# Optimization experiments

Hardware: AMD Instinct MI355X
Metric: run time of the kernel (lower is better)

The kernel has to match this reference:

```python
import jax, jax.numpy as jnp
import numpy as np

# Dims: tokens [B,H,W,C]; 3x3 local window (NB=9 neighbors); relative-pos embed dim RP.
B, H, W, C = 4, 96, 96, 128
K, NB, RP = 3, 9, 8
HID = 128              # edge_hidden_dim = max(hidden_dim//2=128, feature_dim=128)
EDGE_IN = 3 * C + RP   # [center, neighbor, center-neighbor, rel_pos] -> 392
CLIP = 3.0
GATE_EPS = 1e-6
LN_EPS = 1e-5


def _ln(x, w, b):
    m = jnp.mean(x, axis=-1, keepdims=True)
    v = jnp.mean((x - m) ** 2, axis=-1, keepdims=True)
    return (x - m) * jax.lax.rsqrt(v + LN_EPS) * w + b


def _mlp(x, w1, b1, w2, b2):
    # Linear -> GELU (exact/erf, torch default) -> Linear; dropout is identity in eval mode.
    return jax.nn.gelu(x @ w1 + b1, approximate=False) @ w2 + b2


def _eml(drive, resistance, gamma_raw, lam, bias, warmup_eta):
    # EMLUnit energy gate (source not provided; Ohm's-law style drive/resistance,
    # positive resistance via softplus, clipped, warmup-scaled, learned bias).
    gamma = jax.nn.softplus(gamma_raw)
    conduct = drive / (jax.nn.softplus(resistance) + gamma + GATE_EPS)
    return warmup_eta * jnp.clip(lam * conduct, -CLIP, CLIP) + bias


def setup_inputs() -> dict:
    key = jax.random.key(0)
    ks = jax.random.split(key, 8)

    def w(k, shape, std=0.01):
        return jax.random.normal(k, shape, jnp.float32) * std

    return {
        "tokens": jax.random.normal(ks[0], (B, H, W, C), jnp.float32),
        "ln1_w": jnp.ones((C,), jnp.float32), "ln1_b": jnp.zeros((C,), jnp.float32),
        "ln2_w": jnp.ones((C,), jnp.float32), "ln2_b": jnp.zeros((C,), jnp.float32),
        "rel_pos": w(ks[1], (NB, RP), 0.02),
        "d_w1": w(ks[2], (EDGE_IN, HID)), "d_b1": jnp.zeros((HID,), jnp.float32),
        "d_w2": w(ks[3], (HID, 1)), "d_b2": jnp.zeros((1,), jnp.float32),
        "r_w1": w(ks[4], (EDGE_IN, HID)), "r_b1": jnp.zeros((HID,), jnp.float32),
        "r_w2": w(ks[5], (HID, 1)), "r_b2": jnp.zeros((1,), jnp.float32),
        "v_w": w(ks[6], (C, C)), "v_b": jnp.zeros((C,), jnp.float32),
        "o_w": w(ks[7], (C, C)), "o_b": jnp.zeros((C,), jnp.float32),
        "eml_gamma": jnp.full((1,), 0.1, jnp.float32),
        "eml_lam": jnp.ones((1,), jnp.float32),
        "eml_bias": jnp.full((1,), -0.3, jnp.float32),
    }


def reference(tokens, ln1_w, ln1_b, ln2_w, ln2_b, rel_pos,
              d_w1, d_b1, d_w2, d_b2, r_w1, r_b1, r_w2, r_b2,
              v_w, v_b, o_w, o_b, eml_gamma, eml_lam, eml_bias):
    b, h, w_, c = tokens.shape
    hw = h * w_
    norm = _ln(tokens, ln1_w, ln1_b)
    # nn.Unfold(kernel=3, padding=1): zero-pad then gather 3x3 windows (row-major ky,kx order).
    pad = jnp.pad(norm, ((0, 0), (1, 1), (1, 1), (0, 0)))
    neigh = jnp.stack([pad[:, dy:dy + h, dx:dx + w_, :]
                       for dy in range(K) for dx in range(K)], axis=3)  # [B,H,W,9,C]
    neigh = neigh.reshape(b, hw, NB, c)
    center = jnp.broadcast_to(norm.reshape(b, hw, 1, c), (b, hw, NB, c))
    relp = jnp.broadcast_to(rel_pos[None, None], (b, hw, NB, RP))
    edge = jnp.concatenate([center, neigh, center - neigh, relp], axis=-1)  # [B,HW,9,392]
    drive = _mlp(edge, d_w1, d_b1, d_w2, d_b2)[..., 0]        # [B,HW,9]
    resistance = _mlp(edge, r_w1, r_b1, r_w2, r_b2)[..., 0]   # [B,HW,9]
    energy = _eml(drive, resistance, eml_gamma, eml_lam, eml_bias, 1.0)
    gate = jax.nn.sigmoid(energy)[..., None]                  # [B,HW,9,1]
    values = neigh @ v_w + v_b                                # [B,HW,9,C]
    gate_mass = jnp.clip(jnp.sum(gate, axis=2), GATE_EPS, None)  # [B,HW,1]
    message = jnp.sum(gate * values, axis=2) / gate_mass      # [B,HW,C]
    update = (message @ o_w + o_b).reshape(b, h, w_, c)
    return _ln(tokens + update, ln2_w, ln2_b)
```

## Files before the change

kernel.cpp:

```cpp
#include <hip/hip_runtime.h>
#include <stdint.h>

#define NPIX 36864

using bf16x8 = __attribute__((ext_vector_type(8))) short;
using f32x4  = __attribute__((ext_vector_type(4))) float;
using f32x2  = __attribute__((ext_vector_type(2))) float;

__device__ __forceinline__ float bf2f(uint16_t u){
  return __uint_as_float(((uint32_t)u) << 16);
}
__device__ __forceinline__ float bl(uint32_t u){ return __uint_as_float(u << 16); }
__device__ __forceinline__ float bh(uint32_t u){ return __uint_as_float(u & 0xFFFF0000u); }
__device__ __forceinline__ uint16_t f2bf(float f){
  uint32_t u = __float_as_uint(f);
  u += 0x7fffu + ((u >> 16) & 1u);
  return (uint16_t)(u >> 16);
}
__device__ __forceinline__ float ldw(const void* p, int i, bool f32){
  return f32 ? ((const float*)p)[i] : bf2f(((const uint16_t*)p)[i]);
}
__device__ __forceinline__ bool probe_f32(const void* ones_vec){
  return ((const uint32_t*)ones_vec)[0] == 0x3F800000u;
}
__device__ __forceinline__ float softplusf(float x){
  return fmaxf(x, 0.f) + __logf(1.f + __expf(-fabsf(x)));
}
__device__ __forceinline__ f32x2 up2(uint32_t u){
  f32x2 r; r.x = __uint_as_float(u << 16); r.y = __uint_as_float(u & 0xFFFF0000u); return r;
}
__device__ __forceinline__ void sg2(f32x2& acc, uint32_t c, uint32_t n, f32x2 r, f32x2 w){
  f32x2 z = up2(c) + up2(n) + r;
  float sx = __builtin_amdgcn_fmed3f(fmaf(z.x, 0.4255f, 0.5f), 0.f, 1.f);
  float sy = __builtin_amdgcn_fmed3f(fmaf(z.y, 0.4255f, 0.5f), 0.f, 1.f);
  acc.x = fmaf(z.x * sx, w.x, acc.x);
  acc.y = fmaf(z.y * sy, w.y, acc.y);
}

#define LIDX(p, ch) ((p)*128 + ((((ch) >> 3) ^ ((p) & 15)) << 3) + ((ch) & 7))

__global__ __launch_bounds__(256) void pre_kernel(const void* __restrict__ tokens,
                            const void* __restrict__ ln1w, const void* __restrict__ ln1b,
                            const void* __restrict__ dw1, const void* __restrict__ rw1,
                            const void* __restrict__ vw,  const void* __restrict__ relp,
                            const void* __restrict__ db1, const void* __restrict__ rb1,
                            const void* __restrict__ ow,
                            const void* __restrict__ dw2, const void* __restrict__ rw2,
                            const void* __restrict__ vb,  const void* __restrict__ db2,
                            const void* __restrict__ rb2, const void* __restrict__ eg,
                            const void* __restrict__ el,  const void* __restrict__ eb,
                            uint16_t* __restrict__ norm,
                            uint16_t* __restrict__ wcatT, float* __restrict__ Rd,
                            float* __restrict__ Rr, uint16_t* __restrict__ owT,
                            float* __restrict__ w2df, float* __restrict__ w2rf,
                            float* __restrict__ vbf, float* __restrict__ sc){
  const bool F = probe_f32(ln1w);
  const int b = blockIdx.x;
  if (b < NPIX/4){
    const int wv = threadIdx.x >> 6, lane = threadIdx.x & 63;
    const int p = b * 4 + wv;
    float f0, f1;
    if (F){
      const float2 t = ((const float2*)tokens)[(size_t)p*64 + lane];
      f0 = t.x; f1 = t.y;
    } else {
      const uint32_t pk = ((const uint32_t*)tokens)[(size_t)p*64 + lane];
      f0 = bl(pk); f1 = bh(pk);
    }
    float s = f0 + f1;
    #pragma unroll
    for (int m = 1; m < 64; m <<= 1) s += __shfl_xor(s, m, 64);
    const float mean = s * (1.f/128.f);
    const float d0 = f0 - mean, d1 = f1 - mean;
    float q = d0*d0 + d1*d1;
    #pragma unroll
    for (int m = 1; m < 64; m <<= 1) q += __shfl_xor(q, m, 64);
    const float rs = rsqrtf(q * (1.f/128.f) + 1e-5f);
    const float n0 = d0*rs*ldw(ln1w, 2*lane, F)   + ldw(ln1b, 2*lane, F);
    const float n1 = d1*rs*ldw(ln1w, 2*lane+1, F) + ldw(ln1b, 2*lane+1, F);
    ((uint32_t*)(norm + (size_t)p*128))[lane] = (uint32_t)f2bf(n0) | ((uint32_t)f2bf(n1) << 16);
    return;
  }
  const int j = (b - NPIX/4) * 2 + (threadIdx.x >> 7);
  const int c = threadIdx.x & 127;
  if (j < 640){
    float val;
    if (j < 128)      val = ldw(dw1, c*128 + j, F)             + ldw(dw1, (256+c)*128 + j, F);
    else if (j < 256) val = ldw(dw1, (128+c)*128 + (j-128), F) - ldw(dw1, (256+c)*128 + (j-128), F);
    else if (j < 384) val = ldw(rw1, c*128 + (j-256), F)       + ldw(rw1, (256+c)*128 + (j-256), F);
    else if (j < 512) val = ldw(rw1, (128+c)*128 + (j-384), F) - ldw(rw1, (256+c)*128 + (j-384), F);
    else              val = ldw(vw, c*128 + (j-512), F);
    wcatT[j*128 + c] = f2bf(val);
  } else if (j < 649){
    const int k = j - 640;
    float sd = ldw(db1, c, F);
    float sr = ldw(rb1, c, F);
    #pragma unroll
    for (int r = 0; r < 8; ++r){
      float rp = ldw(relp, k*8 + r, F);
      sd += rp * ldw(dw1, (384+r)*128 + c, F);
      sr += rp * ldw(rw1, (384+r)*128 + c, F);
    }
    Rd[k*128 + c] = sd;
    Rr[k*128 + c] = sr;
  } else if (j < 777){
    const int n = j - 649;
    owT[n*128 + c] = f2bf(ldw(ow, c*128 + n, F));
  } else {
    w2df[c] = ldw(dw2, c, F);
    w2rf[c] = ldw(rw2, c, F);
    vbf[c]  = ldw(vb, c, F);
    if (c == 0){
      sc[0] = ldw(db2, 0, F);
      sc[1] = ldw(rb2, 0, F);
      sc[2] = softplusf(ldw(eg, 0, F));
      sc[3] = ldw(el, 0, F);
      sc[4] = ldw(eb, 0, F);
    }
  }
}

__global__ __launch_bounds__(512, 4) void mega_kernel(
    const uint16_t* __restrict__ norm, const uint16_t* __restrict__ wcatT,
    const uint16_t* __restrict__ owT,
    const float* __restrict__ Rd, const float* __restrict__ Rr,
    const float* __restrict__ w2df, const float* __restrict__ w2rf,
    const float* __restrict__ sc, const float* __restrict__ vbf,
    const void* __restrict__ tokens, const void* __restrict__ ob,
    const void* __restrict__ ln2w, const void* __restrict__ ln2b,
    void* __restrict__ out){
  __shared__ __align__(16) char smem[78336];
  uint16_t* const Ns = (uint16_t*)smem;
  uint16_t* const PA = (uint16_t*)(smem + 28672);
  uint16_t* const PB = (uint16_t*)(smem + 57344);
  float*    const drv = (float*)(smem + 73728);
  float*    const gts = (float*)(smem + 76032);
  float*    const U   = (float*)smem;

  const int bid0 = blockIdx.x;
  const int bid  = (bid0 & 7)*72 + (bid0 >> 3);
  const int b  = bid / 144;
  const int tl = bid - b*144;
  const int ty = tl / 12;
  const int y0 = ty*8, x0 = (tl - ty*12)*8;
  const int tid = threadIdx.x;
  const int wv = tid >> 6, lane = tid & 63;
  const int lr = lane & 15, quad = lane >> 4;
  const float sc0 = sc[0], sc1 = sc[1], sc2 = sc[2], sc3 = sc[3], sc4 = sc[4];

  #pragma unroll
  for (int i = 0; i < 4; ++i){
    const int idx = tid + i*512;
    if (idx < 1792){
      const int hq = idx >> 4, g = idx & 15;
      uint4 v = {0u,0u,0u,0u};
      if (hq < 100){
        const int hy = hq/10, hx = hq - hy*10;
        const int y = y0 - 1 + hy, x = x0 - 1 + hx;
        if (((unsigned)y < 96u) && ((unsigned)x < 96u))
          v = *(const uint4*)&norm[((size_t)((b*96+y)*96+x))*128 + g*8];
      }
      *(uint4*)&Ns[hq*128 + ((g ^ (hq & 15)) << 3)] = v;
    }
  }

  auto loadB = [&](const uint16_t* __restrict__ Wp, bf16x8 (&bfr)[4]){
    const uint16_t* base = Wp + (size_t)(wv*16 + lr)*128 + quad*8;
    #pragma unroll
    for (int kk = 0; kk < 4; ++kk)
      bfr[kk] = *(const bf16x8*)(base + kk*32);
  };

  auto gemmH = [&](const uint16_t* __restrict__ Wp){
    bf16x8 bfr[4];
    loadB(Wp, bfr);
    f32x4 acc[7] = {};
    #pragma unroll
    for (int kk = 0; kk < 4; ++kk){
      const int chunk = kk*4 + quad;
      #pragma unroll
      for (int mi = 0; mi < 7; ++mi){
        const int r = mi*16 + lr;
        const bf16x8 a = *(const bf16x8*)&Ns[r*128 + ((chunk ^ (r & 15)) << 3)];
        acc[mi] = __builtin_amdgcn_mfma_f32_16x16x32_bf16(a, bfr[kk], acc[mi], 0, 0, 0);
      }
    }
    const int col = wv*16 + lr;
    #pragma unroll
    for (int mi = 0; mi < 7; ++mi){
      const int rowb = mi*16 + quad*4;
      #pragma unroll
      for (int r = 0; r < 4; ++r)
        PA[LIDX(rowb + r, col)] = f2bf(acc[mi][r]);
    }
  };

  auto gemmC = [&](const uint16_t* __restrict__ Wp){
    bf16x8 bfr[4];
    loadB(Wp, bfr);
    f32x4 acc[4] = {};
    #pragma unroll
    for (int kk = 0; kk < 4; ++kk){
      const int chunk = kk*4 + quad;
      #pragma unroll
      for (int mi = 0; mi < 4; ++mi){
        const int r = mi*16 + lr;
        const int hr = (r >> 3)*10 + (r & 7) + 11;
        const bf16x8 a = *(const bf16x8*)&Ns[hr*128 + ((chunk ^ (hr & 15)) << 3)];
        acc[mi] = __builtin_amdgcn_mfma_f32_16x16x32_bf16(a, bfr[kk], acc[mi], 0, 0, 0);
      }
    }
    const int col = wv*16 + lr;
    #pragma unroll
    for (int mi = 0; mi < 4; ++mi){
      const int rowb = mi*16 + quad*4;
      #pragma unroll
      for (int r = 0; r < 4; ++r)
        PB[LIDX(rowb + r, col)] = f2bf(acc[mi][r]);
    }
  };

  auto edge = [&](const float* __restrict__ Rk, const float* __restrict__ w2, bool isDrive){
    const int pl = lane >> 3, cg = lane & 7;
    for (int i = 0; i < 9; ++i){
      const int it = wv*9 + i;
      const int k = it >> 3, ry = it & 7;
      const int ky = k/3, kx = k - ky*3;
      const int pr = ry*8 + pl;
      const int hq = (ry + ky)*10 + pl + kx;
      const int g0 = 2*cg;
      const uint4 c0 = *(const uint4*)((const char*)PB + pr*256 + (((g0)  ^ (pr & 15)) << 4));
      const uint4 c1 = *(const uint4*)((const char*)PB + pr*256 + (((g0+1)^ (pr & 15)) << 4));
      const uint4 n0 = *(const uint4*)((const char*)PA + hq*256 + (((g0)  ^ (hq & 15)) << 4));
      const uint4 n1 = *(const uint4*)((const char*)PA + hq*256 + (((g0+1)^ (hq & 15)) << 4));
      const float4* r4 = (const float4*)(Rk + k*128) + cg*4;
      const float4* w4 = (const float4*)w2 + cg*4;
      const float4 Ra = r4[0], Rb = r4[1], Rc = r4[2], Rv = r4[3];
      const float4 Wa = w4[0], Wb = w4[1], Wc = w4[2], Wd = w4[3];
      f32x2 a = {0.f, 0.f};
      sg2(a, c0.x, n0.x, f32x2{Ra.x, Ra.y}, f32x2{Wa.x, Wa.y});
      sg2(a, c0.y, n0.y, f32x2{Ra.z, Ra.w}, f32x2{Wa.z, Wa.w});
      sg2(a, c0.z, n0.z, f32x2{Rb.x, Rb.y}, f32x2{Wb.x, Wb.y});
      sg2(a, c0.w, n0.w, f32x2{Rb.z, Rb.w}, f32x2{Wb.z, Wb.w});
      sg2(a, c1.x, n1.x, f32x2{Rc.x, Rc.y}, f32x2{Wc.x, Wc.y});
      sg2(a, c1.y, n1.y, f32x2{Rc.z, Rc.w}, f32x2{Wc.z, Wc.w});
      sg2(a, c1.z, n1.z, f32x2{Rv.x, Rv.y}, f32x2{Wd.x, Wd.y});
      sg2(a, c1.w, n1.w, f32x2{Rv.z, Rv.w}, f32x2{Wd.z, Wd.w});
      float s = a.x + a.y;
      s += __shfl_xor(s, 1, 64); s += __shfl_xor(s, 2, 64); s += __shfl_xor(s, 4, 64);
      if (cg == 0){
        if (isDrive){
          drv[k*64 + pr] = s;
        } else {
          const float drive  = drv[k*64 + pr] + sc0;
          const float resist = s + sc1;
          const float cond = __fdividef(drive, softplusf(resist) + sc2 + 1e-6f);
          const float en = fminf(fmaxf(sc3 * cond, -3.0f), 3.0f) + sc4;
          const float e = __expf(-en);
          gts[k*64 + pr] = __builtin_amdgcn_rcpf(1.0f + e);
        }
      }
    }
  };

  const uint16_t* const W0 = wcatT;
  const uint16_t* const W1 = wcatT + (size_t)1*128*128;
  const uint16_t* const W2 = wcatT + (size_t)2*128*128;
  const uint16_t* const W3 = wcatT + (size_t)3*128*128;
  const uint16_t* const W4 = wcatT + (size_t)4*128*128;

  __syncthreads();
  gemmH(W1); gemmC(W0);
  __syncthreads();
  edge(Rd, w2df, true);
  __syncthreads();
  gemmH(W3); gemmC(W2);
  __syncthreads();
  edge(Rr, w2rf, false);
  __syncthreads();
  gemmH(W4);
  __syncthreads();

  {
    const float2 vb2 = ((const float2*)vbf)[lane];
    const int g = lane >> 2, lb = (lane & 3)*4;
    #pragma unroll
    for (int j = 0; j < 8; ++j){
      const int mp = wv*8 + j;
      const int my = mp >> 3, mx = mp & 7;
      float gk[9], gsum = 0.f;
      #pragma unroll
      for (int kk = 0; kk < 9; ++kk){ gk[kk] = gts[kk*64 + mp]; gsum += gk[kk]; }
      float a0 = 0.f, a1 = 0.f;
      #pragma unroll
      for (int kk = 0; kk < 9; ++kk){
        const int kyy = kk / 3;
        const int h2  = (my + kyy)*10 + (mx + kk - kyy*3);
        const uint32_t u = *(const uint32_t*)((const char*)PA + h2*256 + ((g ^ (h2 & 15)) << 4) + lb);
        a0 = fmaf(gk[kk], bl(u), a0);
        a1 = fmaf(gk[kk], bh(u), a1);
      }
      const float inv = __fdividef(1.0f, fmaxf(gsum, 1e-6f));
      a0 = (a0 + gsum * vb2.x) * inv;
      a1 = (a1 + gsum * vb2.y) * inv;
      *(uint32_t*)((char*)PB + mp*256 + ((g ^ (mp & 15)) << 4) + lb) =
          (uint32_t)f2bf(a0) | ((uint32_t)f2bf(a1) << 16);
    }
  }
  __syncthreads();

  f32x4 acc[4] = {};
  {
    bf16x8 bfr[4];
    loadB(owT, bfr);
    #pragma unroll
    for (int kk = 0; kk < 4; ++kk){
      const int chunk = kk*4 + quad;
      #pragma unroll
      for (int mi = 0; mi < 4; ++mi){
        const int r = mi*16 + lr;
        const bf16x8 a = *(const bf16x8*)&PB[r*128 + ((chunk ^ (r & 15)) << 3)];
        acc[mi] = __builtin_amdgcn_mfma_f32_16x16x32_bf16(a, bfr[kk], acc[mi], 0, 0, 0);
      }
    }
  }
  __syncthreads();
  {
    const int col = wv*16 + lr;
    #pragma unroll
    for (int mi = 0; mi < 4; ++mi)
      #pragma unroll
      for (int r = 0; r < 4; ++r)
        U[(mi*16 + quad*4 + r)*128 + col] = acc[mi][r];
  }
  __syncthreads();

  const bool F = probe_f32(ln2w);
  const float lw0 = ldw(ln2w, 2*lane, F), lw1 = ldw(ln2w, 2*lane+1, F);
  const float lb0 = ldw(ln2b, 2*lane, F), lb1 = ldw(ln2b, 2*lane+1, F);
  const float ob0 = ldw(ob, 2*lane, F),   ob1 = ldw(ob, 2*lane+1, F);
  #pragma unroll
  for (int j = 0; j < 8; ++j){
    const int row = wv*8 + j;
    const int my = row >> 3, mx = row & 7;
    const size_t p = (size_t)((b*96 + y0 + my)*96 + (x0 + mx));
    const float2 uv = ((const float2*)U)[row*64 + lane];
    float t0, t1;
    if (F){
      const float2 tk = ((const float2*)tokens)[p*64 + lane];
      t0 = tk.x; t1 = tk.y;
    } else {
      const uint32_t tk = ((const uint32_t*)tokens)[p*64 + lane];
      t0 = bl(tk); t1 = bh(tk);
    }
    const float a0 = uv.x + ob0 + t0;
    const float a1 = uv.y + ob1 + t1;
    float s = a0 + a1;
    #pragma unroll
    for (int m = 1; m < 64; m <<= 1) s += __shfl_xor(s, m, 64);
    const float mean = s * (1.f/128.f);
    const float d0 = a0 - mean, d1 = a1 - mean;
    float q = d0*d0 + d1*d1;
    #pragma unroll
    for (int m = 1; m < 64; m <<= 1) q += __shfl_xor(q, m, 64);
    const float rs = rsqrtf(q * (1.f/128.f) + 1e-5f);
    const float o0 = d0*rs*lw0 + lb0;
    const float o1 = d1*rs*lw1 + lb1;
    if (F){
      ((float2*)out)[p*64 + lane] = make_float2(o0, o1);
    } else {
      ((uint32_t*)out)[p*64 + lane] = (uint32_t)f2bf(o0) | ((uint32_t)f2bf(o1) << 16);
    }
  }
}

extern "C" void kernel_launch(void* const* d_in, const int* in_sizes, int n_in,
                              void* d_out, int out_size, void* d_ws, size_t ws_size,
                              hipStream_t stream) {
  const void* tokens = d_in[0];
  const void* ln1w   = d_in[1];
  const void* ln1b   = d_in[2];
  const void* ln2w   = d_in[3];
  const void* ln2b   = d_in[4];
  const void* relp   = d_in[5];
  const void* dw1    = d_in[6];
  const void* db1    = d_in[7];
  const void* dw2    = d_in[8];
  const void* db2    = d_in[9];
  const void* rw1    = d_in[10];
  const void* rb1    = d_in[11];
  const void* rw2    = d_in[12];
  const void* rb2    = d_in[13];
  const void* vw     = d_in[14];
  const void* vb     = d_in[15];
  const void* ow     = d_in[16];
  const void* ob     = d_in[17];
  const void* eg     = d_in[18];
  const void* el     = d_in[19];
  const void* eb     = d_in[20];

  char* ws = (char*)d_ws;
  uint16_t* normb = (uint16_t*)(ws + 0);
  uint16_t* wcatT = (uint16_t*)(ws + 9437184);
  float*    Rd    = (float*)   (ws + 9601024);
  float*    Rr    = (float*)   (ws + 9605632);
  uint16_t* owT   = (uint16_t*)(ws + 9610240);
  float*    w2df  = (float*)   (ws + 9643008);
  float*    w2rf  = (float*)   (ws + 9643520);
  float*    vbf   = (float*)   (ws + 9644032);
  float*    sc    = (float*)   (ws + 9644544);

  pre_kernel<<<NPIX/4 + 389, 256, 0, stream>>>(tokens, ln1w, ln1b,
                                       dw1, rw1, vw, relp, db1, rb1, ow,
                                       dw2, rw2, vb, db2, rb2, eg, el, eb,
                                       normb, wcatT, Rd, Rr, owT, w2df, w2rf, vbf, sc);
  mega_kernel<<<576, 512, 0, stream>>>(normb, wcatT, owT, Rd, Rr, w2df, w2rf,
                                       sc, vbf, tokens, ob, ln2w, ln2b, d_out);
}
```

Measured before the change: 187.5 us.

## Halve spatial tile to 4x8 pixels with 256-thread blocks and 2-column-tile waves

Shrinks each block's tile from 8x8 to 4x8 pixels and uses 256 threads instead of 512, doubling the grid to 1152 blocks. LDS use drops from about 78 KB to about 43 KB per block. Each wave now computes two 16-column MFMA tiles, reusing each A fragment across both. The aim is more resident blocks and better load balance across CUs, at the cost of a larger halo fraction (6x10 halo rows for 32 pixels) and more redundant neighbor GEMM work per pixel.

```diff
diff --git a/kernel.cpp b/kernel.cpp
--- a/kernel.cpp
+++ b/kernel.cpp
@@ -120,7 +120,7 @@
   }
 }
 
-__global__ __launch_bounds__(512, 4) void mega_kernel(
+__global__ __launch_bounds__(256, 3) void mega_kernel(
     const uint16_t* __restrict__ norm, const uint16_t* __restrict__ wcatT,
     const uint16_t* __restrict__ owT,
     const float* __restrict__ Rd, const float* __restrict__ Rr,
@@ -129,20 +129,20 @@
     const void* __restrict__ tokens, const void* __restrict__ ob,
     const void* __restrict__ ln2w, const void* __restrict__ ln2b,
     void* __restrict__ out){
-  __shared__ __align__(16) char smem[78336];
+  __shared__ __align__(16) char smem[43264];
   uint16_t* const Ns = (uint16_t*)smem;
-  uint16_t* const PA = (uint16_t*)(smem + 28672);
-  uint16_t* const PB = (uint16_t*)(smem + 57344);
-  float*    const drv = (float*)(smem + 73728);
-  float*    const gts = (float*)(smem + 76032);
+  uint16_t* const PA = (uint16_t*)(smem + 16384);
+  uint16_t* const PB = (uint16_t*)(smem + 32768);
+  float*    const drv = (float*)(smem + 40960);
+  float*    const gts = (float*)(smem + 42112);
   float*    const U   = (float*)smem;
 
   const int bid0 = blockIdx.x;
-  const int bid  = (bid0 & 7)*72 + (bid0 >> 3);
-  const int b  = bid / 144;
-  const int tl = bid - b*144;
+  const int bid  = (bid0 & 7)*144 + (bid0 >> 3);
+  const int b  = bid / 288;
+  const int tl = bid - b*288;
   const int ty = tl / 12;
-  const int y0 = ty*8, x0 = (tl - ty*12)*8;
+  const int y0 = ty*4, x0 = (tl - ty*12)*8;
   const int tid = threadIdx.x;
   const int wv = tid >> 6, lane = tid & 63;
   const int lr = lane & 15, quad = lane >> 4;
@@ -150,73 +150,84 @@
 
   #pragma unroll
   for (int i = 0; i < 4; ++i){
-    const int idx = tid + i*512;
-    if (idx < 1792){
-      const int hq = idx >> 4, g = idx & 15;
-      uint4 v = {0u,0u,0u,0u};
-      if (hq < 100){
-        const int hy = hq/10, hx = hq - hy*10;
-        const int y = y0 - 1 + hy, x = x0 - 1 + hx;
-        if (((unsigned)y < 96u) && ((unsigned)x < 96u))
-          v = *(const uint4*)&norm[((size_t)((b*96+y)*96+x))*128 + g*8];
-      }
-      *(uint4*)&Ns[hq*128 + ((g ^ (hq & 15)) << 3)] = v;
-    }
-  }
-
-  auto loadB = [&](const uint16_t* __restrict__ Wp, bf16x8 (&bfr)[4]){
-    const uint16_t* base = Wp + (size_t)(wv*16 + lr)*128 + quad*8;
-    #pragma unroll
-    for (int kk = 0; kk < 4; ++kk)
-      bfr[kk] = *(const bf16x8*)(base + kk*32);
+    const int idx = tid + i*256;
+    const int hq = idx >> 4, g = idx & 15;
+    uint4 v = {0u,0u,0u,0u};
+    if (hq < 60){
+      const int hy = hq/10, hx = hq - hy*10;
+      const int y = y0 - 1 + hy, x = x0 - 1 + hx;
+      if (((unsigned)y < 96u) && ((unsigned)x < 96u))
+        v = *(const uint4*)&norm[((size_t)((b*96+y)*96+x))*128 + g*8];
+    }
+    *(uint4*)&Ns[hq*128 + ((g ^ (hq & 15)) << 3)] = v;
+  }
+
+  auto loadB = [&](const uint16_t* __restrict__ Wp, bf16x8 (&bfr)[2][4]){
+    #pragma unroll
+    for (int ni = 0; ni < 2; ++ni){
+      const uint16_t* base = Wp + (size_t)(wv*32 + ni*16 + lr)*128 + quad*8;
+      #pragma unroll
+      for (int kk = 0; kk < 4; ++kk)
+        bfr[ni][kk] = *(const bf16x8*)(base + kk*32);
+    }
   };
 
   auto gemmH = [&](const uint16_t* __restrict__ Wp){
-    bf16x8 bfr[4];
+    bf16x8 bfr[2][4];
     loadB(Wp, bfr);
-    f32x4 acc[7] = {};
+    f32x4 acc[4][2] = {};
     #pragma unroll
     for (int kk = 0; kk < 4; ++kk){
       const int chunk = kk*4 + quad;
       #pragma unroll
-      for (int mi = 0; mi < 7; ++mi){
+      for (int mi = 0; mi < 4; ++mi){
         const int r = mi*16 + lr;
         const bf16x8 a = *(const bf16x8*)&Ns[r*128 + ((chunk ^ (r & 15)) << 3)];
-        acc[mi] = __builtin_amdgcn_mfma_f32_16x16x32_bf16(a, bfr[kk], acc[mi], 0, 0, 0);
-      }
-    }
-    const int col = wv*16 + lr;
-    #pragma unroll
-    for (int mi = 0; mi < 7; ++mi){
-      const int rowb = mi*16 + quad*4;
-      #pragma unroll
-      for (int r = 0; r < 4; ++r)
-        PA[LIDX(rowb + r, col)] = f2bf(acc[mi][r]);
+        #pragma unroll
+        for (int ni = 0; ni < 2; ++ni)
+          acc[mi][ni] = __builtin_amdgcn_mfma_f32_16x16x32_bf16(a, bfr[ni][kk], acc[mi][ni], 0, 0, 0);
+      }
+    }
+    #pragma unroll
+    for (int mi = 0; mi < 4; ++mi){
+      #pragma unroll
+      for (int ni = 0; ni < 2; ++ni){
+        const int ch   = wv*32 + ni*16 + lr;
+        const int rowb = mi*16 + quad*4;
+        #pragma unroll
+        for (int r = 0; r < 4; ++r)
+          PA[LIDX(rowb + r, ch)] = f2bf(acc[mi][ni][r]);
+      }
     }
   };
 
   auto gemmC = [&](const uint16_t* __restrict__ Wp){
-    bf16x8 bfr[4];
+    bf16x8 bfr[2][4];
     loadB(Wp, bfr);
-    f32x4 acc[4] = {};
+    f32x4 acc[2][2] = {};
     #pragma unroll
     for (int kk = 0; kk < 4; ++kk){
       const int chunk = kk*4 + quad;
       #pragma unroll
-      for (int mi = 0; mi < 4; ++mi){
+      for (int mi = 0; mi < 2; ++mi){
         const int r = mi*16 + lr;
         const int hr = (r >> 3)*10 + (r & 7) + 11;
         const bf16x8 a = *(const bf16x8*)&Ns[hr*128 + ((chunk ^ (hr & 15)) << 3)];
-        acc[mi] = __builtin_amdgcn_mfma_f32_16x16x32_bf16(a, bfr[kk], acc[mi], 0, 0, 0);
-      }
-    }
-    const int col = wv*16 + lr;
-    #pragma unroll
-    for (int mi = 0; mi < 4; ++mi){
-      const int rowb = mi*16 + quad*4;
-      #pragma unroll
-      for (int r = 0; r < 4; ++r)
-        PB[LIDX(rowb + r, col)] = f2bf(acc[mi][r]);
+        #pragma unroll
+        for (int ni = 0; ni < 2; ++ni)
+          acc[mi][ni] = __builtin_amdgcn_mfma_f32_16x16x32_bf16(a, bfr[ni][kk], acc[mi][ni], 0, 0, 0);
+      }
+    }
+    #pragma unroll
+    for (int mi = 0; mi < 2; ++mi){
+      #pragma unroll
+      for (int ni = 0; ni < 2; ++ni){
+        const int ch   = wv*32 + ni*16 + lr;
+        const int rowb = mi*16 + quad*4;
+        #pragma unroll
+        for (int r = 0; r < 4; ++r)
+          PB[LIDX(rowb + r, ch)] = f2bf(acc[mi][ni][r]);
+      }
     }
   };
 
@@ -224,7 +235,7 @@
     const int pl = lane >> 3, cg = lane & 7;
     for (int i = 0; i < 9; ++i){
       const int it = wv*9 + i;
-      const int k = it >> 3, ry = it & 7;
+      const int k = it >> 2, ry = it & 3;
       const int ky = k/3, kx = k - ky*3;
       const int pr = ry*8 + pl;
       const int hq = (ry + ky)*10 + pl + kx;
@@ -250,14 +261,14 @@
       s += __shfl_xor(s, 1, 64); s += __shfl_xor(s, 2, 64); s += __shfl_xor(s, 4, 64);
       if (cg == 0){
         if (isDrive){
-          drv[k*64 + pr] = s;
+          drv[k*32 + pr] = s;
         } else {
-          const float drive  = drv[k*64 + pr] + sc0;
+          const float drive  = drv[k*32 + pr] + sc0;
           const float resist = s + sc1;
           const float cond = __fdividef(drive, softplusf(resist) + sc2 + 1e-6f);
           const float en = fminf(fmaxf(sc3 * cond, -3.0f), 3.0f) + sc4;
           const float e = __expf(-en);
-          gts[k*64 + pr] = __builtin_amdgcn_rcpf(1.0f + e);
+          gts[k*32 + pr] = __builtin_amdgcn_rcpf(1.0f + e);
         }
       }
     }
@@ -290,7 +301,7 @@
       const int my = mp >> 3, mx = mp & 7;
       float gk[9], gsum = 0.f;
       #pragma unroll
-      for (int kk = 0; kk < 9; ++kk){ gk[kk] = gts[kk*64 + mp]; gsum += gk[kk]; }
+      for (int kk = 0; kk < 9; ++kk){ gk[kk] = gts[kk*32 + mp]; gsum += gk[kk]; }
       float a0 = 0.f, a1 = 0.f;
       #pragma unroll
       for (int kk = 0; kk < 9; ++kk){
@@ -309,29 +320,34 @@
   }
   __syncthreads();
 
-  f32x4 acc[4] = {};
+  f32x4 acc[2][2] = {};
   {
-    bf16x8 bfr[4];
+    bf16x8 bfr[2][4];
     loadB(owT, bfr);
     #pragma unroll
     for (int kk = 0; kk < 4; ++kk){
       const int chunk = kk*4 + quad;
       #pragma unroll
-      for (int mi = 0; mi < 4; ++mi){
+      for (int mi = 0; mi < 2; ++mi){
         const int r = mi*16 + lr;
         const bf16x8 a = *(const bf16x8*)&PB[r*128 + ((chunk ^ (r & 15)) << 3)];
-        acc[mi] = __builtin_amdgcn_mfma_f32_16x16x32_bf16(a, bfr[kk], acc[mi], 0, 0, 0);
+        #pragma unroll
+        for (int ni = 0; ni < 2; ++ni)
+          acc[mi][ni] = __builtin_amdgcn_mfma_f32_16x16x32_bf16(a, bfr[ni][kk], acc[mi][ni], 0, 0, 0);
       }
     }
   }
   __syncthreads();
   {
-    const int col = wv*16 + lr;
-    #pragma unroll
-    for (int mi = 0; mi < 4; ++mi)
-      #pragma unroll
-      for (int r = 0; r < 4; ++r)
-        U[(mi*16 + quad*4 + r)*128 + col] = acc[mi][r];
+    #pragma unroll
+    for (int mi = 0; mi < 2; ++mi)
+      #pragma unroll
+      for (int ni = 0; ni < 2; ++ni){
+        const int col = wv*32 + ni*16 + lr;
+        #pragma unroll
+        for (int r = 0; r < 4; ++r)
+          U[(mi*16 + quad*4 + r)*128 + col] = acc[mi][ni][r];
+      }
   }
   __syncthreads();
 
@@ -414,6 +430,6 @@
                                        dw1, rw1, vw, relp, db1, rb1, ow,
                                        dw2, rw2, vb, db2, rb2, eg, el, eb,
                                        normb, wcatT, Rd, Rr, owT, w2df, w2rf, vbf, sc);
-  mega_kernel<<<576, 512, 0, stream>>>(normb, wcatT, owT, Rd, Rr, w2df, w2rf,
-                                       sc, vbf, tokens, ob, ln2w, ln2b, d_out);
-}
+  mega_kernel<<<1152, 256, 0, stream>>>(normb, wcatT, owT, Rd, Rr, w2df, w2rf,
+                                        sc, vbf, tokens, ob, ln2w, ln2b, d_out);
+}
```

Measured after the change: 189.0 us. No clear change (+0.8%).

## Reuse center features across neighbors in edge loop and batch LN1 pixels

Applied to the files above, without the earlier changes.

The edge stage now assigns each wave one row of 8 pixels and loops over the 9 neighbors. The center features and second-layer weights are loaded and unpacked once per wave, and the next neighbor's LDS reads are prefetched while the current one is computed. The LN1 pre-kernel handles two pixels per wave so that shuffle reductions interleave, and it launches half as many blocks. The drive and gate buffers share one LDS region, and a barrier before the U write-back is removed because U does not overlap the PB region the preceding MFMA loop reads.

```diff
diff --git a/kernel.cpp b/kernel.cpp
--- a/kernel.cpp
+++ b/kernel.cpp
@@ -29,10 +29,11 @@
 __device__ __forceinline__ f32x2 up2(uint32_t u){
   f32x2 r; r.x = __uint_as_float(u << 16); r.y = __uint_as_float(u & 0xFFFF0000u); return r;
 }
-__device__ __forceinline__ void sg2(f32x2& acc, uint32_t c, uint32_t n, f32x2 r, f32x2 w){
-  f32x2 z = up2(c) + up2(n) + r;
-  float sx = __builtin_amdgcn_fmed3f(fmaf(z.x, 0.4255f, 0.5f), 0.f, 1.f);
-  float sy = __builtin_amdgcn_fmed3f(fmaf(z.y, 0.4255f, 0.5f), 0.f, 1.f);
+__device__ __forceinline__ void sgf(f32x2& acc, f32x2 c, uint32_t n, f32x2 r, f32x2 w){
+  const f32x2 nf = up2(n);
+  f32x2 z; z.x = c.x + nf.x + r.x; z.y = c.y + nf.y + r.y;
+  const float sx = __builtin_amdgcn_fmed3f(fmaf(z.x, 0.4255f, 0.5f), 0.f, 1.f);
+  const float sy = __builtin_amdgcn_fmed3f(fmaf(z.y, 0.4255f, 0.5f), 0.f, 1.f);
   acc.x = fmaf(z.x * sx, w.x, acc.x);
   acc.y = fmaf(z.y * sy, w.y, acc.y);
 }
@@ -56,32 +57,38 @@
                             float* __restrict__ vbf, float* __restrict__ sc){
   const bool F = probe_f32(ln1w);
   const int b = blockIdx.x;
-  if (b < NPIX/4){
+  if (b < NPIX/8){
     const int wv = threadIdx.x >> 6, lane = threadIdx.x & 63;
-    const int p = b * 4 + wv;
-    float f0, f1;
+    const int p = b * 8 + wv * 2;
+    float a0, a1, c0, c1;
     if (F){
-      const float2 t = ((const float2*)tokens)[(size_t)p*64 + lane];
-      f0 = t.x; f1 = t.y;
+      const float2 ta = ((const float2*)tokens)[(size_t)p*64 + lane];
+      const float2 tb = ((const float2*)tokens)[(size_t)(p+1)*64 + lane];
+      a0 = ta.x; a1 = ta.y; c0 = tb.x; c1 = tb.y;
     } else {
-      const uint32_t pk = ((const uint32_t*)tokens)[(size_t)p*64 + lane];
-      f0 = bl(pk); f1 = bh(pk);
-    }
-    float s = f0 + f1;
-    #pragma unroll
-    for (int m = 1; m < 64; m <<= 1) s += __shfl_xor(s, m, 64);
-    const float mean = s * (1.f/128.f);
-    const float d0 = f0 - mean, d1 = f1 - mean;
-    float q = d0*d0 + d1*d1;
-    #pragma unroll
-    for (int m = 1; m < 64; m <<= 1) q += __shfl_xor(q, m, 64);
-    const float rs = rsqrtf(q * (1.f/128.f) + 1e-5f);
-    const float n0 = d0*rs*ldw(ln1w, 2*lane, F)   + ldw(ln1b, 2*lane, F);
-    const float n1 = d1*rs*ldw(ln1w, 2*lane+1, F) + ldw(ln1b, 2*lane+1, F);
-    ((uint32_t*)(norm + (size_t)p*128))[lane] = (uint32_t)f2bf(n0) | ((uint32_t)f2bf(n1) << 16);
+      const uint32_t ua = ((const uint32_t*)tokens)[(size_t)p*64 + lane];
+      const uint32_t ub = ((const uint32_t*)tokens)[(size_t)(p+1)*64 + lane];
+      a0 = bl(ua); a1 = bh(ua); c0 = bl(ub); c1 = bh(ub);
+    }
+    float sa = a0 + a1, sb = c0 + c1;
+    #pragma unroll
+    for (int m = 1; m < 64; m <<= 1){ sa += __shfl_xor(sa, m, 64); sb += __shfl_xor(sb, m, 64); }
+    const float ma = sa * (1.f/128.f), mb = sb * (1.f/128.f);
+    const float da0 = a0 - ma, da1 = a1 - ma, db0 = c0 - mb, db1 = c1 - mb;
+    float qa = da0*da0 + da1*da1, qb = db0*db0 + db1*db1;
+    #pragma unroll
+    for (int m = 1; m < 64; m <<= 1){ qa += __shfl_xor(qa, m, 64); qb += __shfl_xor(qb, m, 64); }
+    const float ra = rsqrtf(qa * (1.f/128.f) + 1e-5f);
+    const float rb = rsqrtf(qb * (1.f/128.f) + 1e-5f);
+    const float w0 = ldw(ln1w, 2*lane, F), w1 = ldw(ln1w, 2*lane+1, F);
+    const float bb0 = ldw(ln1b, 2*lane, F), bb1 = ldw(ln1b, 2*lane+1, F);
+    const float na0 = da0*ra*w0 + bb0, na1 = da1*ra*w1 + bb1;
+    const float nb0 = db0*rb*w0 + bb0, nb1 = db1*rb*w1 + bb1;
+    ((uint32_t*)(norm + (size_t)p*128))[lane]     = (uint32_t)f2bf(na0) | ((uint32_t)f2bf(na1) << 16);
+    ((uint32_t*)(norm + (size_t)(p+1)*128))[lane] = (uint32_t)f2bf(nb0) | ((uint32_t)f2bf(nb1) << 16);
     return;
   }
-  const int j = (b - NPIX/4) * 2 + (threadIdx.x >> 7);
+  const int j = (b - NPIX/8) * 2 + (threadIdx.x >> 7);
   const int c = threadIdx.x & 127;
   if (j < 640){
     float val;
@@ -129,13 +136,12 @@
     const void* __restrict__ tokens, const void* __restrict__ ob,
     const void* __restrict__ ln2w, const void* __restrict__ ln2b,
     void* __restrict__ out){
-  __shared__ __align__(16) char smem[78336];
+  __shared__ __align__(16) char smem[76032];
   uint16_t* const Ns = (uint16_t*)smem;
   uint16_t* const PA = (uint16_t*)(smem + 28672);
   uint16_t* const PB = (uint16_t*)(smem + 57344);
-  float*    const drv = (float*)(smem + 73728);
-  float*    const gts = (float*)(smem + 76032);
-  float*    const U   = (float*)smem;
+  float*    const dg = (float*)(smem + 73728);
+  float*    const U  = (float*)smem;
 
   const int bid0 = blockIdx.x;
   const int bid  = (bid0 & 7)*72 + (bid0 >> 3);
@@ -222,42 +228,49 @@
 
   auto edge = [&](const float* __restrict__ Rk, const float* __restrict__ w2, bool isDrive){
     const int pl = lane >> 3, cg = lane & 7;
-    for (int i = 0; i < 9; ++i){
-      const int it = wv*9 + i;
-      const int k = it >> 3, ry = it & 7;
-      const int ky = k/3, kx = k - ky*3;
-      const int pr = ry*8 + pl;
-      const int hq = (ry + ky)*10 + pl + kx;
-      const int g0 = 2*cg;
-      const uint4 c0 = *(const uint4*)((const char*)PB + pr*256 + (((g0)  ^ (pr & 15)) << 4));
-      const uint4 c1 = *(const uint4*)((const char*)PB + pr*256 + (((g0+1)^ (pr & 15)) << 4));
-      const uint4 n0 = *(const uint4*)((const char*)PA + hq*256 + (((g0)  ^ (hq & 15)) << 4));
-      const uint4 n1 = *(const uint4*)((const char*)PA + hq*256 + (((g0+1)^ (hq & 15)) << 4));
+    const int pr = wv*8 + pl;
+    const int g0 = 2*cg;
+    const uint4 c0 = *(const uint4*)((const char*)PB + pr*256 + (((g0)  ^ (pr & 15)) << 4));
+    const uint4 c1 = *(const uint4*)((const char*)PB + pr*256 + (((g0+1)^ (pr & 15)) << 4));
+    const f32x2 cf0 = up2(c0.x), cf1 = up2(c0.y), cf2 = up2(c0.z), cf3 = up2(c0.w);
+    const f32x2 cf4 = up2(c1.x), cf5 = up2(c1.y), cf6 = up2(c1.z), cf7 = up2(c1.w);
+    const float4* w4 = (const float4*)w2 + cg*4;
+    const float4 Wa = w4[0], Wb = w4[1], Wc = w4[2], Wd = w4[3];
+    const int h0 = wv*10 + pl;
+    uint4 n0 = *(const uint4*)((const char*)PA + h0*256 + (((g0)  ^ (h0 & 15)) << 4));
+    uint4 n1 = *(const uint4*)((const char*)PA + h0*256 + (((g0+1)^ (h0 & 15)) << 4));
+    for (int k = 0; k < 9; ++k){
+      const uint4 m0 = n0, m1 = n1;
+      if (k < 8){
+        const int k2 = k + 1;
+        const int ky2 = k2 / 3, kx2 = k2 - ky2*3;
+        const int h2 = (wv + ky2)*10 + pl + kx2;
+        n0 = *(const uint4*)((const char*)PA + h2*256 + (((g0)  ^ (h2 & 15)) << 4));
+        n1 = *(const uint4*)((const char*)PA + h2*256 + (((g0+1)^ (h2 & 15)) << 4));
+      }
       const float4* r4 = (const float4*)(Rk + k*128) + cg*4;
-      const float4* w4 = (const float4*)w2 + cg*4;
       const float4 Ra = r4[0], Rb = r4[1], Rc = r4[2], Rv = r4[3];
-      const float4 Wa = w4[0], Wb = w4[1], Wc = w4[2], Wd = w4[3];
       f32x2 a = {0.f, 0.f};
-      sg2(a, c0.x, n0.x, f32x2{Ra.x, Ra.y}, f32x2{Wa.x, Wa.y});
-      sg2(a, c0.y, n0.y, f32x2{Ra.z, Ra.w}, f32x2{Wa.z, Wa.w});
-      sg2(a, c0.z, n0.z, f32x2{Rb.x, Rb.y}, f32x2{Wb.x, Wb.y});
-      sg2(a, c0.w, n0.w, f32x2{Rb.z, Rb.w}, f32x2{Wb.z, Wb.w});
-      sg2(a, c1.x, n1.x, f32x2{Rc.x, Rc.y}, f32x2{Wc.x, Wc.y});
-      sg2(a, c1.y, n1.y, f32x2{Rc.z, Rc.w}, f32x2{Wc.z, Wc.w});
-      sg2(a, c1.z, n1.z, f32x2{Rv.x, Rv.y}, f32x2{Wd.x, Wd.y});
-      sg2(a, c1.w, n1.w, f32x2{Rv.z, Rv.w}, f32x2{Wd.z, Wd.w});
+      sgf(a, cf0, m0.x, f32x2{Ra.x, Ra.y}, f32x2{Wa.x, Wa.y});
+      sgf(a, cf1, m0.y, f32x2{Ra.z, Ra.w}, f32x2{Wa.z, Wa.w});
+      sgf(a, cf2, m0.z, f32x2{Rb.x, Rb.y}, f32x2{Wb.x, Wb.y});
+      sgf(a, cf3, m0.w, f32x2{Rb.z, Rb.w}, f32x2{Wb.z, Wb.w});
+      sgf(a, cf4, m1.x, f32x2{Rc.x, Rc.y}, f32x2{Wc.x, Wc.y});
+      sgf(a, cf5, m1.y, f32x2{Rc.z, Rc.w}, f32x2{Wc.z, Wc.w});
+      sgf(a, cf6, m1.z, f32x2{Rv.x, Rv.y}, f32x2{Wd.x, Wd.y});
+      sgf(a, cf7, m1.w, f32x2{Rv.z, Rv.w}, f32x2{Wd.z, Wd.w});
       float s = a.x + a.y;
       s += __shfl_xor(s, 1, 64); s += __shfl_xor(s, 2, 64); s += __shfl_xor(s, 4, 64);
       if (cg == 0){
         if (isDrive){
-          drv[k*64 + pr] = s;
+          dg[k*64 + pr] = s;
         } else {
-          const float drive  = drv[k*64 + pr] + sc0;
+          const float drive  = dg[k*64 + pr] + sc0;
           const float resist = s + sc1;
           const float cond = __fdividef(drive, softplusf(resist) + sc2 + 1e-6f);
           const float en = fminf(fmaxf(sc3 * cond, -3.0f), 3.0f) + sc4;
           const float e = __expf(-en);
-          gts[k*64 + pr] = __builtin_amdgcn_rcpf(1.0f + e);
+          dg[k*64 + pr] = __builtin_amdgcn_rcpf(1.0f + e);
         }
       }
     }
@@ -290,7 +303,7 @@
       const int my = mp >> 3, mx = mp & 7;
       float gk[9], gsum = 0.f;
       #pragma unroll
-      for (int kk = 0; kk < 9; ++kk){ gk[kk] = gts[kk*64 + mp]; gsum += gk[kk]; }
+      for (int kk = 0; kk < 9; ++kk){ gk[kk] = dg[kk*64 + mp]; gsum += gk[kk]; }
       float a0 = 0.f, a1 = 0.f;
       #pragma unroll
       for (int kk = 0; kk < 9; ++kk){
@@ -324,7 +337,6 @@
       }
     }
   }
-  __syncthreads();
   {
     const int col = wv*16 + lr;
     #pragma unroll
@@ -410,7 +422,7 @@
   float*    vbf   = (float*)   (ws + 9644032);
   float*    sc    = (float*)   (ws + 9644544);
 
-  pre_kernel<<<NPIX/4 + 389, 256, 0, stream>>>(tokens, ln1w, ln1b,
+  pre_kernel<<<NPIX/8 + 389, 256, 0, stream>>>(tokens, ln1w, ln1b,
                                        dw1, rw1, vw, relp, db1, rb1, ow,
                                        dw2, rw2, vb, db2, rb2, eg, el, eb,
                                        normb, wcatT, Rd, Rr, owT, w2df, w2rf, vbf, sc);
```

Measured after the change: 189.5 us. No clear change (+1.0%).

## Fuse LayerNorm1 into mega kernel and drop the normalized-token workspace

Applied to the files above, without the earlier changes.

Moves the first LayerNorm out of the pre-pass and into the main tile kernel. Each block now normalizes its own 10x10 halo directly from the tokens and writes bf16 results into shared memory. This removes the 9.4MB normalized-token write and re-read and the 9216 extra pre-kernel blocks, and shrinks the pre-kernel to weight preparation only. In exchange, halo pixels are normalized redundantly (about 1.56x recompute, with shuffle reductions per row). The change also merges the drive and gate shared buffers to cut LDS use and removes one barrier before the U store.

```diff
diff --git a/kernel.cpp b/kernel.cpp
--- a/kernel.cpp
+++ b/kernel.cpp
@@ -39,8 +39,8 @@
 
 #define LIDX(p, ch) ((p)*128 + ((((ch) >> 3) ^ ((p) & 15)) << 3) + ((ch) & 7))
 
-__global__ __launch_bounds__(256) void pre_kernel(const void* __restrict__ tokens,
-                            const void* __restrict__ ln1w, const void* __restrict__ ln1b,
+__global__ __launch_bounds__(256) void pre_kernel(
+                            const void* __restrict__ ln1w,
                             const void* __restrict__ dw1, const void* __restrict__ rw1,
                             const void* __restrict__ vw,  const void* __restrict__ relp,
                             const void* __restrict__ db1, const void* __restrict__ rb1,
@@ -49,39 +49,12 @@
                             const void* __restrict__ vb,  const void* __restrict__ db2,
                             const void* __restrict__ rb2, const void* __restrict__ eg,
                             const void* __restrict__ el,  const void* __restrict__ eb,
-                            uint16_t* __restrict__ norm,
                             uint16_t* __restrict__ wcatT, float* __restrict__ Rd,
                             float* __restrict__ Rr, uint16_t* __restrict__ owT,
                             float* __restrict__ w2df, float* __restrict__ w2rf,
                             float* __restrict__ vbf, float* __restrict__ sc){
   const bool F = probe_f32(ln1w);
-  const int b = blockIdx.x;
-  if (b < NPIX/4){
-    const int wv = threadIdx.x >> 6, lane = threadIdx.x & 63;
-    const int p = b * 4 + wv;
-    float f0, f1;
-    if (F){
-      const float2 t = ((const float2*)tokens)[(size_t)p*64 + lane];
-      f0 = t.x; f1 = t.y;
-    } else {
-      const uint32_t pk = ((const uint32_t*)tokens)[(size_t)p*64 + lane];
-      f0 = bl(pk); f1 = bh(pk);
-    }
-    float s = f0 + f1;
-    #pragma unroll
-    for (int m = 1; m < 64; m <<= 1) s += __shfl_xor(s, m, 64);
-    const float mean = s * (1.f/128.f);
-    const float d0 = f0 - mean, d1 = f1 - mean;
-    float q = d0*d0 + d1*d1;
-    #pragma unroll
-    for (int m = 1; m < 64; m <<= 1) q += __shfl_xor(q, m, 64);
-    const float rs = rsqrtf(q * (1.f/128.f) + 1e-5f);
-    const float n0 = d0*rs*ldw(ln1w, 2*lane, F)   + ldw(ln1b, 2*lane, F);
-    const float n1 = d1*rs*ldw(ln1w, 2*lane+1, F) + ldw(ln1b, 2*lane+1, F);
-    ((uint32_t*)(norm + (size_t)p*128))[lane] = (uint32_t)f2bf(n0) | ((uint32_t)f2bf(n1) << 16);
-    return;
-  }
-  const int j = (b - NPIX/4) * 2 + (threadIdx.x >> 7);
+  const int j = blockIdx.x * 2 + (threadIdx.x >> 7);
   const int c = threadIdx.x & 127;
   if (j < 640){
     float val;
@@ -121,21 +94,21 @@
 }
 
 __global__ __launch_bounds__(512, 4) void mega_kernel(
-    const uint16_t* __restrict__ norm, const uint16_t* __restrict__ wcatT,
+    const void* __restrict__ tokens, const uint16_t* __restrict__ wcatT,
     const uint16_t* __restrict__ owT,
     const float* __restrict__ Rd, const float* __restrict__ Rr,
     const float* __restrict__ w2df, const float* __restrict__ w2rf,
     const float* __restrict__ sc, const float* __restrict__ vbf,
-    const void* __restrict__ tokens, const void* __restrict__ ob,
+    const void* __restrict__ ln1w, const void* __restrict__ ln1b,
+    const void* __restrict__ ob,
     const void* __restrict__ ln2w, const void* __restrict__ ln2b,
     void* __restrict__ out){
-  __shared__ __align__(16) char smem[78336];
+  __shared__ __align__(16) char smem[76032];
   uint16_t* const Ns = (uint16_t*)smem;
   uint16_t* const PA = (uint16_t*)(smem + 28672);
   uint16_t* const PB = (uint16_t*)(smem + 57344);
-  float*    const drv = (float*)(smem + 73728);
-  float*    const gts = (float*)(smem + 76032);
-  float*    const U   = (float*)smem;
+  float*    const dg = (float*)(smem + 73728);
+  float*    const U  = (float*)smem;
 
   const int bid0 = blockIdx.x;
   const int bid  = (bid0 & 7)*72 + (bid0 >> 3);
@@ -147,20 +120,44 @@
   const int wv = tid >> 6, lane = tid & 63;
   const int lr = lane & 15, quad = lane >> 4;
   const float sc0 = sc[0], sc1 = sc[1], sc2 = sc[2], sc3 = sc[3], sc4 = sc[4];
-
-  #pragma unroll
-  for (int i = 0; i < 4; ++i){
-    const int idx = tid + i*512;
-    if (idx < 1792){
-      const int hq = idx >> 4, g = idx & 15;
-      uint4 v = {0u,0u,0u,0u};
+  const bool F = probe_f32(ln1w);
+
+  {
+    const float w0 = ldw(ln1w, 2*lane, F), w1 = ldw(ln1w, 2*lane+1, F);
+    const float bb0 = ldw(ln1b, 2*lane, F), bb1 = ldw(ln1b, 2*lane+1, F);
+    #pragma unroll
+    for (int r = 0; r < 14; ++r){
+      const int hq = wv + r*8;
+      uint32_t wword = 0u;
       if (hq < 100){
         const int hy = hq/10, hx = hq - hy*10;
         const int y = y0 - 1 + hy, x = x0 - 1 + hx;
-        if (((unsigned)y < 96u) && ((unsigned)x < 96u))
-          v = *(const uint4*)&norm[((size_t)((b*96+y)*96+x))*128 + g*8];
-      }
-      *(uint4*)&Ns[hq*128 + ((g ^ (hq & 15)) << 3)] = v;
+        if (((unsigned)y < 96u) && ((unsigned)x < 96u)){
+          const size_t p = (size_t)((b*96 + y)*96 + x);
+          float f0, f1;
+          if (F){
+            const float2 t = ((const float2*)tokens)[p*64 + lane];
+            f0 = t.x; f1 = t.y;
+          } else {
+            const uint32_t pk = ((const uint32_t*)tokens)[p*64 + lane];
+            f0 = bl(pk); f1 = bh(pk);
+          }
+          float s = f0 + f1;
+          #pragma unroll
+          for (int m = 1; m < 64; m <<= 1) s += __shfl_xor(s, m, 64);
+          const float mean = s * (1.f/128.f);
+          const float d0 = f0 - mean, d1 = f1 - mean;
+          float q = d0*d0 + d1*d1;
+          #pragma unroll
+          for (int m = 1; m < 64; m <<= 1) q += __shfl_xor(q, m, 64);
+          const float rs = rsqrtf(q * (1.f/128.f) + 1e-5f);
+          const float n0 = d0*rs*w0 + bb0;
+          const float n1 = d1*rs*w1 + bb1;
+          wword = (uint32_t)f2bf(n0) | ((uint32_t)f2bf(n1) << 16);
+        }
+      }
+      const int g = lane >> 2;
+      *(uint32_t*)&Ns[hq*128 + ((g ^ (hq & 15)) << 3) + ((2*lane) & 7)] = wword;
     }
   }
 
@@ -250,14 +247,14 @@
       s += __shfl_xor(s, 1, 64); s += __shfl_xor(s, 2, 64); s += __shfl_xor(s, 4, 64);
       if (cg == 0){
         if (isDrive){
-          drv[k*64 + pr] = s;
+          dg[k*64 + pr] = s;
         } else {
-          const float drive  = drv[k*64 + pr] + sc0;
+          const float drive  = dg[k*64 + pr] + sc0;
           const float resist = s + sc1;
           const float cond = __fdividef(drive, softplusf(resist) + sc2 + 1e-6f);
           const float en = fminf(fmaxf(sc3 * cond, -3.0f), 3.0f) + sc4;
           const float e = __expf(-en);
-          gts[k*64 + pr] = __builtin_amdgcn_rcpf(1.0f + e);
+          dg[k*64 + pr] = __builtin_amdgcn_rcpf(1.0f + e);
         }
       }
     }
@@ -290,7 +287,7 @@
       const int my = mp >> 3, mx = mp & 7;
       float gk[9], gsum = 0.f;
       #pragma unroll
-      for (int kk = 0; kk < 9; ++kk){ gk[kk] = gts[kk*64 + mp]; gsum += gk[kk]; }
+      for (int kk = 0; kk < 9; ++kk){ gk[kk] = dg[kk*64 + mp]; gsum += gk[kk]; }
       float a0 = 0.f, a1 = 0.f;
       #pragma unroll
       for (int kk = 0; kk < 9; ++kk){
@@ -324,7 +321,6 @@
       }
     }
   }
-  __syncthreads();
   {
     const int col = wv*16 + lr;
     #pragma unroll
@@ -335,7 +331,6 @@
   }
   __syncthreads();
 
-  const bool F = probe_f32(ln2w);
   const float lw0 = ldw(ln2w, 2*lane, F), lw1 = ldw(ln2w, 2*lane+1, F);
   const float lb0 = ldw(ln2b, 2*lane, F), lb1 = ldw(ln2b, 2*lane+1, F);
   const float ob0 = ldw(ob, 2*lane, F),   ob1 = ldw(ob, 2*lane+1, F);
@@ -400,20 +395,19 @@
   const void* eb     = d_in[20];
 
   char* ws = (char*)d_ws;
-  uint16_t* normb = (uint16_t*)(ws + 0);
-  uint16_t* wcatT = (uint16_t*)(ws + 9437184);
-  float*    Rd    = (float*)   (ws + 9601024);
-  float*    Rr    = (float*)   (ws + 9605632);
-  uint16_t* owT   = (uint16_t*)(ws + 9610240);
-  float*    w2df  = (float*)   (ws + 9643008);
-  float*    w2rf  = (float*)   (ws + 9643520);
-  float*    vbf   = (float*)   (ws + 9644032);
-  float*    sc    = (float*)   (ws + 9644544);
-
-  pre_kernel<<<NPIX/4 + 389, 256, 0, stream>>>(tokens, ln1w, ln1b,
-                                       dw1, rw1, vw, relp, db1, rb1, ow,
-                                       dw2, rw2, vb, db2, rb2, eg, el, eb,
-                                       normb, wcatT, Rd, Rr, owT, w2df, w2rf, vbf, sc);
-  mega_kernel<<<576, 512, 0, stream>>>(normb, wcatT, owT, Rd, Rr, w2df, w2rf,
-                                       sc, vbf, tokens, ob, ln2w, ln2b, d_out);
-}
+  uint16_t* wcatT = (uint16_t*)(ws + 0);
+  float*    Rd    = (float*)   (ws + 163840);
+  float*    Rr    = (float*)   (ws + 168448);
+  uint16_t* owT   = (uint16_t*)(ws + 173056);
+  float*    w2df  = (float*)   (ws + 205824);
+  float*    w2rf  = (float*)   (ws + 206336);
+  float*    vbf   = (float*)   (ws + 206848);
+  float*    sc    = (float*)   (ws + 207360);
+
+  pre_kernel<<<389, 256, 0, stream>>>(ln1w,
+                                      dw1, rw1, vw, relp, db1, rb1, ow,
+                                      dw2, rw2, vb, db2, rb2, eg, el, eb,
+                                      wcatT, Rd, Rr, owT, w2df, w2rf, vbf, sc);
+  mega_kernel<<<576, 512, 0, stream>>>(tokens, wcatT, owT, Rd, Rr, w2df, w2rf,
+                                       sc, vbf, ln1w, ln1b, ob, ln2w, ln2b, d_out);
+}
```

After: 195.9 us. +4.5%, slower.
